# Kernel tuning notes

Hardware: AMD Instinct MI355X
Metric: run time of the kernel (lower is better)

The kernel has to match this reference:

```python
import jax, jax.numpy as jnp
import numpy as np

B, H, W, C = 8, 64, 64, 128
G = 8
K = 3
STRIDE, PAD, DIL = 1, 1, 1
OS = 1.0
HID = 2 * C
C_OUT = C
EPS = 1e-5


def setup_inputs():
    key = jax.random.key(0)
    ks = jax.random.split(key, 16)

    def n(k, shape, s=0.02):
        return jax.random.normal(k, shape, dtype=jnp.float32) * s

    inp = jax.random.normal(ks[0], (B, H, W, C), dtype=jnp.float32)
    return {
        "inp": inp,
        "w_proj": n(ks[1], (C, C), 0.05),
        "b_proj": jnp.zeros((C,), jnp.float32),
        "dw_w": n(ks[2], (C, 1, K, K), 0.1),
        "dw_b": jnp.zeros((C,), jnp.float32),
        "gamma": jnp.ones((C,), jnp.float32),
        "beta": jnp.zeros((C,), jnp.float32),
        "w_off": n(ks[3], (G * K * K * 2, C), 0.02),
        "b_off": n(ks[4], (G * K * K * 2,), 0.02),
        "w_mask": n(ks[5], (G * K * K, C), 0.02),
        "b_mask": n(ks[6], (G * K * K,), 0.02),
        "w_fc1": n(ks[7], (HID, C), 0.05),
        "b_fc1": jnp.zeros((HID,), jnp.float32),
        "w_fc2": n(ks[8], (C_OUT, HID), 0.05),
        "b_fc2": jnp.zeros((C_OUT,), jnp.float32),
    }


def _dcnv3_core(x, offset, mask):
    # x: (B,H,W,C); offset: (B,H,W,G*P*2); mask: (B,H,W,G*P), softmaxed over P
    b, h, w, c = x.shape
    cg = c // G
    p = K * K
    xpad = jnp.pad(x, ((0, 0), (PAD, PAD), (PAD, PAD), (0, 0)))
    hp, wp = h + 2 * PAD, w + 2 * PAD
    hout = (hp - (DIL * (K - 1) + 1)) // STRIDE + 1
    wout = (wp - (DIL * (K - 1) + 1)) // STRIDE + 1
    # reference points, normalized by padded spatial dims (DCNv3 convention)
    base = (DIL * (K - 1)) // 2 + 0.5
    ref_y = (base + jnp.arange(hout, dtype=x.dtype) * STRIDE) / hp
    ref_x = (base + jnp.arange(wout, dtype=x.dtype) * STRIDE) / wp
    # dilation kernel grid; flatten with p = i*K + j (row-major over kernel)
    k_lin = jnp.arange(K, dtype=x.dtype) * DIL - (DIL * (K - 1)) // 2
    grid_y = jnp.repeat(k_lin / hp, K)   # (P,)
    grid_x = jnp.tile(k_lin / wp, K)     # (P,)
    off = offset.reshape(b, hout, wout, G, p, 2)  # last dim = (dx, dy)
    loc_x = ref_x[None, None, :, None, None] + grid_x * OS + off[..., 0] * OS / wp
    loc_y = ref_y[None, :, None, None, None] + grid_y * OS + off[..., 1] * OS / hp
    # normalized [0,1] -> pixel coords (grid_sample align_corners=False)
    px = loc_x * wp - 0.5
    py = loc_y * hp - 0.5
    x0 = jnp.floor(px)
    y0 = jnp.floor(py)
    wx = px - x0
    wy = py - y0
    x0i = x0.astype(jnp.int32)
    y0i = y0.astype(jnp.int32)
    xg = xpad.reshape(b, hp * wp, G, cg).transpose(0, 2, 1, 3)  # (B,G,HpWp,Cg)
    m_tot = hout * wout * p

    def bgp(t):  # (B,Hout,Wout,G,P) -> (B,G,M,1)
        return t.transpose(0, 3, 1, 2, 4).reshape(b, G, m_tot)[..., None]

    def gather(iy, ix):
        valid = ((iy >= 0) & (iy < hp) & (ix >= 0) & (ix < wp)).astype(x.dtype)
        flat = jnp.clip(iy, 0, hp - 1) * wp + jnp.clip(ix, 0, wp - 1)
        v = jnp.take_along_axis(xg, bgp(flat), axis=2)  # (B,G,M,Cg)
        return v * bgp(valid)  # zero padding outside

    wxr, wyr = bgp(wx), bgp(wy)
    val = (gather(y0i, x0i) * (1 - wyr) * (1 - wxr)
           + gather(y0i, x0i + 1) * (1 - wyr) * wxr
           + gather(y0i + 1, x0i) * wyr * (1 - wxr)
           + gather(y0i + 1, x0i + 1) * wyr * wxr)
    m = bgp(mask.reshape(b, hout, wout, G, p))
    out = (val * m).reshape(b, G, hout * wout, p, cg).sum(3)  # (B,G,N,Cg)
    return out.transpose(0, 2, 1, 3).reshape(b, hout, wout, G * cg)


def reference(inp, w_proj, b_proj, dw_w, dw_b, gamma, beta, w_off, b_off,
              w_mask, b_mask, w_fc1, b_fc1, w_fc2, b_fc2):
    bsz = inp.shape[0]
    x = inp @ w_proj.T + b_proj  # input_proj
    # offset/mask branch: depthwise conv -> BN (batch stats) -> GELU
    xc = inp.transpose(0, 3, 1, 2)  # NCHW
    y = jax.lax.conv_general_dilated(
        xc, dw_w, (1, 1), [((K - 1) // 2, (K - 1) // 2)] * 2,
        feature_group_count=C, dimension_numbers=("NCHW", "OIHW", "NCHW"))
    y = y + dw_b[None, :, None, None]
    mean = y.mean(axis=(0, 2, 3), keepdims=True)
    var = ((y - mean) ** 2).mean(axis=(0, 2, 3), keepdims=True)
    y = (y - mean) * jax.lax.rsqrt(var + EPS)
    y = y * gamma[None, :, None, None] + beta[None, :, None, None]
    x1 = jax.nn.gelu(y, approximate=False).transpose(0, 2, 3, 1)  # (B,H,W,C)
    offset = x1 @ w_off.T + b_off
    mask = x1 @ w_mask.T + b_mask
    mask = jax.nn.softmax(mask.reshape(bsz, H, W, G, K * K), axis=-1).reshape(bsz, H, W, -1)
    x = _dcnv3_core(x, offset, mask)
    # out_proj MLP
    hdn = jax.nn.gelu(x @ w_fc1.T + b_fc1, approximate=False)
    out = hdn @ w_fc2.T + b_fc2
    return out.transpose(0, 3, 1, 2)  # (B,C_out,H,W)
```

## Files before the change

kernel.cpp:

```cpp
#include <hip/hip_runtime.h>
#include <math.h>

#define NPOS  32768
#define CDIM  128
#define HS    64
#define WSZ   64

typedef __bf16 bf8_t  __attribute__((ext_vector_type(8)));
typedef float  f32x4  __attribute__((ext_vector_type(4)));

__device__ __forceinline__ float gelu_exact(float x) {
    return 0.5f * x * (1.0f + erff(x * 0.70710678118654752f));
}

__device__ __forceinline__ unsigned short bf16c(float v) {
    return __builtin_bit_cast(unsigned short, (__bf16)v);
}

__device__ __forceinline__ uint4 pack8hi(const float* v) {
    unsigned hh[8];
    #pragma unroll
    for (int i = 0; i < 8; ++i) hh[i] = (unsigned)bf16c(v[i]);
    return make_uint4(hh[0] | (hh[1] << 16), hh[2] | (hh[3] << 16),
                      hh[4] | (hh[5] << 16), hh[6] | (hh[7] << 16));
}

__device__ __forceinline__ float bfd(unsigned u) {
    return __builtin_bit_cast(float, u << 16);
}

__device__ __forceinline__ void ufma(float* acc, uint4 c, float wgt) {
    const unsigned* cc = (const unsigned*)&c;
    #pragma unroll
    for (int j = 0; j < 4; ++j) {
        acc[2 * j]     += __builtin_bit_cast(float, cc[j] << 16) * wgt;
        acc[2 * j + 1] += __builtin_bit_cast(float, cc[j] & 0xFFFF0000u) * wgt;
    }
}


__device__ void prep_body(
    int bid, int tid,
    unsigned short* __restrict__ xpad,
    const float* __restrict__ w0, const float* __restrict__ w1,
    const float* __restrict__ w2, const float* __restrict__ w3,
    const float* __restrict__ w4, unsigned short* __restrict__ wb)
{
    if (bid < 130) {
        int idx = bid * 256 + tid;
        if (idx < 33280) {
            int c8 = (idx & 15) * 8;
            int cell = idx >> 4;
            int b = cell / 260, r = cell % 260;
            int h, w;
            if (r < 66)       { h = 0;  w = r; }
            else if (r < 132) { h = 65; w = r - 66; }
            else { int rr = r - 132; h = 1 + (rr >> 1); w = (rr & 1) * 65; }
            size_t o = (((size_t)b * 66 + h) * 66 + w) * 128 + c8;
            *(uint4*)(xpad + o) = make_uint4(0u, 0u, 0u, 0u);
        }
    } else {
        int sub = (bid - 130) * 4 + (tid >> 6);
        int lane = tid & 63;
        int NT, K, local; unsigned short* out; bool hl; bool comb = false;
        const float* W = nullptr; int N = 0;
        if (sub < 32)       { NT = 8;  K = 128; out = wb;          local = sub;       hl = false; W = w0; N = 128; }
        else if (sub < 88)  { NT = 14; K = 128; out = wb + 16384;  local = sub - 32;  hl = false; comb = true; }
        else if (sub < 152) { NT = 16; K = 128; out = wb + 45056;  local = sub - 88;  hl = true;  W = w3; N = 256; }
        else                { NT = 8;  K = 256; out = wb + 110592; local = sub - 152; hl = true;  W = w4; N = 128; }
        int KC = K / 32;
        int unit = KC * NT * 512;
        int kc = local / NT, t = local % NT;
        int nt = t * 16 + (lane & 15);
        const float* Wp = W; int n = nt, Nv = N;
        if (comb) {
            if (t < 9) { Wp = w1; n = nt;       Nv = 144; }
            else       { Wp = w2; n = nt - 144; Nv = 72;  }
        }
        int kb = kc * 32 + (lane >> 4) * 8;
        size_t base = ((size_t)local * 64 + lane) * 8;
        #pragma unroll
        for (int i = 0; i < 8; ++i) {
            float v = (n < Nv) ? Wp[(size_t)n * K + kb + i] : 0.f;
            __bf16 h = (__bf16)v;
            out[base + i] = __builtin_bit_cast(unsigned short, h);
            if (hl) {
                __bf16 l = (__bf16)(v - (float)h);
                out[unit + base + i] = __builtin_bit_cast(unsigned short, l);
            }
        }
    }
}

__device__ void dwconv_body(
    int blk, int tid,
    const float* __restrict__ inp, const float* __restrict__ dww,
    const float* __restrict__ dwb, unsigned short* __restrict__ ydwb,
    float* __restrict__ psum, float* __restrict__ psq,
    unsigned short* __restrict__ inpf)
{
    int b = blk >> 6, h = blk & 63;
    int c4 = (tid & 31) * 4;
    int wg = tid >> 5;

    float wreg[4][9];
    #pragma unroll
    for (int cc = 0; cc < 4; ++cc)
        #pragma unroll
        for (int p = 0; p < 9; ++p)
            wreg[cc][p] = dww[(c4 + cc) * 9 + p];
    float bia[4];
    #pragma unroll
    for (int cc = 0; cc < 4; ++cc) bia[cc] = dwb[c4 + cc];

    float s4[4] = {0,0,0,0}, q4[4] = {0,0,0,0};
    const float* ibase = inp + (size_t)(b << 12) * CDIM;

    for (int i = 0; i < 8; ++i) {
        int w = wg + i * 8;
        float acc[4] = {bia[0], bia[1], bia[2], bia[3]};
        float4 ctr;
        #pragma unroll
        for (int ky = 0; ky < 3; ++ky) {
            int yy = h + ky - 1;
            if (yy < 0 || yy >= HS) continue;
            #pragma unroll
            for (int kx = 0; kx < 3; ++kx) {
                int xx = w + kx - 1;
                if (xx < 0 || xx >= WSZ) continue;
                float4 v = *(const float4*)(ibase + (size_t)(yy * 64 + xx) * CDIM + c4);
                if (ky == 1 && kx == 1) ctr = v;
                int p = ky * 3 + kx;
                acc[0] += v.x * wreg[0][p];
                acc[1] += v.y * wreg[1][p];
                acc[2] += v.z * wreg[2][p];
                acc[3] += v.w * wreg[3][p];
            }
        }
        int r = (b << 12) + h * 64 + w;
        ushort4 o;
        o.x = bf16c(acc[0]); o.y = bf16c(acc[1]);
        o.z = bf16c(acc[2]); o.w = bf16c(acc[3]);
        *(ushort4*)(ydwb + (size_t)r * CDIM + c4) = o;
        {
            int rt = r >> 4, kc = c4 >> 5;
            int lp = (r & 15) + ((c4 & 31) >> 3) * 16;
            int i0 = c4 & 7;
            unsigned u0 = (unsigned)bf16c(ctr.x) | ((unsigned)bf16c(ctr.y) << 16);
            unsigned u1 = (unsigned)bf16c(ctr.z) | ((unsigned)bf16c(ctr.w) << 16);
            *(uint2*)(inpf + ((size_t)rt * 4 + kc) * 512 + lp * 8 + i0) = make_uint2(u0, u1);
        }
        #pragma unroll
        for (int cc = 0; cc < 4; ++cc) { s4[cc] += acc[cc]; q4[cc] += acc[cc] * acc[cc]; }
    }

    __shared__ float ls[8][128], lq[8][128];
    #pragma unroll
    for (int cc = 0; cc < 4; ++cc) { ls[wg][c4 + cc] = s4[cc]; lq[wg][c4 + cc] = q4[cc]; }
    __syncthreads();
    if (tid < 128) {
        float s = 0.f, q = 0.f;
        #pragma unroll
        for (int r = 0; r < 8; ++r) { s += ls[r][tid]; q += lq[r][tid]; }
        psum[blk * 128 + tid] = s;
        psq [blk * 128 + tid] = q;
    }
}

__global__ __launch_bounds__(256) void k_pd(
    const float* __restrict__ inp, unsigned short* __restrict__ inpf,
    unsigned short* __restrict__ xpad,
    const float* __restrict__ w0, const float* __restrict__ w1,
    const float* __restrict__ w2, const float* __restrict__ w3,
    const float* __restrict__ w4, unsigned short* __restrict__ wb,
    const float* __restrict__ dww, const float* __restrict__ dwb,
    unsigned short* __restrict__ ydwb, float* __restrict__ psum,
    float* __restrict__ psq)
{
    int bid = blockIdx.x;
    if (bid < 184) prep_body(bid, threadIdx.x, xpad, w0, w1, w2, w3, w4, wb);
    else           dwconv_body(bid - 184, threadIdx.x, inp, dww, dwb, ydwb, psum, psq, inpf);
}

__global__ __launch_bounds__(256) void k_bnstats(
    const float* __restrict__ psum, const float* __restrict__ psq,
    const float* __restrict__ gamma, const float* __restrict__ beta,
    float* __restrict__ sc, float* __restrict__ sh)
{
    int c = blockIdx.x;
    int t = threadIdx.x;
    float s = psum[t * 128 + c] + psum[(t + 256) * 128 + c];
    float q = psq [t * 128 + c] + psq [(t + 256) * 128 + c];
    __shared__ float rs[256], rq[256];
    rs[t] = s; rq[t] = q; __syncthreads();
    for (int off = 128; off > 0; off >>= 1) {
        if (t < off) { rs[t] += rs[t + off]; rq[t] += rq[t + off]; }
        __syncthreads();
    }
    if (t == 0) {
        float mean = rs[0] * (1.0f / 32768.0f);
        float var  = rq[0] * (1.0f / 32768.0f) - mean * mean;
        float scale = gamma[c] * rsqrtf(var + 1e-5f);
        sc[c] = scale;
        sh[c] = beta[c] - mean * scale;
    }
}

__device__ void bngelu_body(
    int bid, int tid,
    const unsigned short* __restrict__ ydwb, const float* __restrict__ sc,
    const float* __restrict__ sh, unsigned short* __restrict__ dst)
{
    int idx = bid * 256 + tid;
    int r = idx >> 4, k8 = (idx & 15) * 8;
    uint4 yv = *(const uint4*)(ydwb + (size_t)r * 128 + k8);
    const unsigned* cc = (const unsigned*)&yv;
    float t[8];
    #pragma unroll
    for (int j = 0; j < 4; ++j) {
        t[2 * j]     = bfd(cc[j]);
        t[2 * j + 1] = __builtin_bit_cast(float, cc[j] & 0xFFFF0000u);
    }
    float s[8], h[8];
    *(float4*)(s)     = *(const float4*)(sc + k8);
    *(float4*)(s + 4) = *(const float4*)(sc + k8 + 4);
    *(float4*)(h)     = *(const float4*)(sh + k8);
    *(float4*)(h + 4) = *(const float4*)(sh + k8 + 4);
    #pragma unroll
    for (int i = 0; i < 8; ++i) t[i] = gelu_exact(t[i] * s[i] + h[i]);
    uint4 hi = pack8hi(t);
    int rt = r >> 4, kc = k8 >> 5, lp = (r & 15) + ((k8 & 31) >> 3) * 16;
    size_t base = ((size_t)rt * 4 + kc) * 512 + lp * 8;
    *(uint4*)(dst + base) = hi;
}

template<int KDIM, int NT_TOT, int NT_W, int MODE, int NV>
__device__ void fgemm_body(
    int bx, int by, int tid,
    const unsigned short* __restrict__ AF, const unsigned short* __restrict__ WF,
    const float* __restrict__ bias, float* __restrict__ C)
{
    constexpr int KC = KDIM / 32;
    int lane = tid & 63, w = tid >> 6;
    int rt0 = bx * 8 + w * 2;
    int t0 = by * NT_W;

    f32x4 acc[2][NT_W];
    #pragma unroll
    for (int rt = 0; rt < 2; ++rt)
        #pragma unroll
        for (int t = 0; t < NT_W; ++t) acc[rt][t] = (f32x4){0.f, 0.f, 0.f, 0.f};

    const bf8_t* Ab0 = (const bf8_t*)AF + (size_t)rt0 * KC * 64 + lane;
    const bf8_t* Ab1 = Ab0 + KC * 64;
    const bf8_t* WHp = (const bf8_t*)WF + lane;

    #pragma unroll
    for (int kc = 0; kc < KC; ++kc) {
        bf8_t a0h = Ab0[kc * 64];
        bf8_t a1h = Ab1[kc * 64];
        #pragma unroll
        for (int t = 0; t < NT_W; ++t) {
            int tg = t0 + t;
            if (tg < NT_TOT) {
                bf8_t wh = WHp[(kc * NT_TOT + tg) * 64];
                acc[0][t] = __builtin_amdgcn_mfma_f32_16x16x32_bf16(wh, a0h, acc[0][t], 0, 0, 0);
                acc[1][t] = __builtin_amdgcn_mfma_f32_16x16x32_bf16(wh, a1h, acc[1][t], 0, 0, 0);
            }
        }
    }

    #pragma unroll
    for (int rt = 0; rt < 2; ++rt) {
        if (MODE == 3) {
            unsigned short* Cp = (unsigned short*)C;
            int m = (rt0 + rt) * 16 + (lane & 15);
            int bb_ = m >> 12, hwm = m & 4095;
            size_t rowb = (((size_t)bb_ * 66 + (hwm >> 6) + 1) * 66 + (hwm & 63) + 1) * 128;
            #pragma unroll
            for (int t = 0; t < NT_W; ++t) {
                int tg = t0 + t;
                int nb = tg * 16 + ((lane >> 4) << 2);
                if (tg < NT_TOT) {
                    float4 bb = *(const float4*)(bias + nb);
                    f32x4 a = acc[rt][t];
                    ushort4 v;
                    v.x = bf16c(a[0] + bb.x); v.y = bf16c(a[1] + bb.y);
                    v.z = bf16c(a[2] + bb.z); v.w = bf16c(a[3] + bb.w);
                    *(ushort4*)(Cp + rowb + nb) = v;
                }
            }
        }
    }
}

__global__ __launch_bounds__(256) void k_bp(
    const unsigned short* __restrict__ ydwb, const float* __restrict__ sc,
    const float* __restrict__ sh, unsigned short* __restrict__ x1f,
    const unsigned short* __restrict__ inpf, const unsigned short* __restrict__ wprojf,
    const float* __restrict__ bproj, unsigned short* __restrict__ xpad)
{
    int bid = blockIdx.x;
    if (bid < 2048) {
        bngelu_body(bid, threadIdx.x, ydwb, sc, sh, x1f);
    } else {
        int pbid = bid - 2048;
        fgemm_body<128, 8, 4, 3, 128>(pbid & 255, pbid >> 8, threadIdx.x,
            inpf, wprojf, bproj, (float*)xpad);
    }
}

__global__ __launch_bounds__(512) void k_dcn(
    const unsigned short* __restrict__ x1f, const unsigned short* __restrict__ womb,
    const float* __restrict__ boff, const float* __restrict__ bmask,
    const unsigned short* __restrict__ xpad, unsigned short* __restrict__ dcnf)
{
    __shared__ unsigned short offs_l[32][148];
    __shared__ unsigned short msk_l[32][76];
    int tid = threadIdx.x;
    int lane = tid & 63, wv = tid >> 6;
    int rtl = wv & 1, chunk = wv >> 1;
    int rt = blockIdx.x * 2 + rtl;

    {
        f32x4 acc[4];
        #pragma unroll
        for (int t = 0; t < 4; ++t) acc[t] = (f32x4){0.f, 0.f, 0.f, 0.f};
        const bf8_t* Ab = (const bf8_t*)x1f + (size_t)rt * 4 * 64 + lane;
        const bf8_t* WH = (const bf8_t*)womb + lane;
        #pragma unroll
        for (int kc = 0; kc < 4; ++kc) {
            bf8_t ah = Ab[kc * 64];
            #pragma unroll
            for (int t = 0; t < 4; ++t) {
                int tg = chunk * 4 + t;
                if (tg < 14) {
                    bf8_t wh = WH[(kc * 14 + tg) * 64];
                    acc[t] = __builtin_amdgcn_mfma_f32_16x16x32_bf16(wh, ah, acc[t], 0, 0, 0);
                }
            }
        }
        int m = rtl * 16 + (lane & 15);
        #pragma unroll
        for (int t = 0; t < 4; ++t) {
            int tg = chunk * 4 + t;
            if (tg < 14) {
                int nb = tg * 16 + ((lane >> 4) << 2);
                f32x4 a = acc[t];
                if (nb < 144) {
                    float4 bb = *(const float4*)(boff + nb);
                    ushort4 v;
                    v.x = bf16c(a[0] + bb.x); v.y = bf16c(a[1] + bb.y);
                    v.z = bf16c(a[2] + bb.z); v.w = bf16c(a[3] + bb.w);
                    *(ushort4*)(&offs_l[m][nb]) = v;
                } else {
                    int col = nb - 144;
                    if (col + 4 <= 72) {
                        float4 bb = *(const float4*)(bmask + col);
                        ushort4 v;
                        v.x = bf16c(a[0] + bb.x); v.y = bf16c(a[1] + bb.y);
                        v.z = bf16c(a[2] + bb.z); v.w = bf16c(a[3] + bb.w);
                        *(ushort4*)(&msk_l[m][col]) = v;
                    }
                }
            }
        }
    }
    __syncthreads();

    int q = tid & 1;
    int g = (tid >> 1) & 7;
    int lpos = tid >> 4;
    int pos = blockIdx.x * 32 + lpos;
    int b = pos >> 12, hw = pos & 4095, h = hw >> 6, w = hw & 63;

    float e[9];
    float mx = -1e30f;
    #pragma unroll
    for (int p = 0; p < 9; ++p) { e[p] = bfd((unsigned)msk_l[lpos][g * 9 + p]); mx = fmaxf(mx, e[p]); }
    float ssum = 0.f;
    #pragma unroll
    for (int p = 0; p < 9; ++p) { e[p] = __expf(e[p] - mx); ssum += e[p]; }
    float inv = 1.0f / ssum;

    int ch = g * 16 + q * 8;
    const unsigned short* xb = xpad + (size_t)b * 557568 + ch;

    float acc[8];
    #pragma unroll
    for (int i = 0; i < 8; ++i) acc[i] = 0.f;

    #pragma unroll
    for (int p = 0; p < 9; ++p) {
        unsigned dpair = *(const unsigned*)(&offs_l[lpos][g * 18 + p * 2]);
        float dx = bfd(dpair);
        float dy = __builtin_bit_cast(float, dpair & 0xFFFF0000u);
        float px = (float)(w + (p % 3)) + dx;
        float py = (float)(h + (p / 3)) + dy;
        float x0f = floorf(px), y0f = floorf(py);
        float wx = px - x0f, wy = py - y0f;
        int ix = (int)x0f, iy = (int)y0f;
        int ix0 = max(min(ix, 65), 0),     ix1 = max(min(ix + 1, 65), 0);
        int iy0 = max(min(iy, 65), 0),     iy1 = max(min(iy + 1, 65), 0);
        int r0 = iy0 * 66, r1 = iy1 * 66;

        float mp  = e[p] * inv;
        float w11 = wy * wx * mp;
        float w10 = wy * mp - w11;
        float w01 = wx * mp - w11;
        float w00 = mp - w01 - w10 - w11;

        uint4 s00 = *(const uint4*)(xb + (size_t)(r0 + ix0) * 128);
        uint4 s01 = *(const uint4*)(xb + (size_t)(r0 + ix1) * 128);
        uint4 s10 = *(const uint4*)(xb + (size_t)(r1 + ix0) * 128);
        uint4 s11 = *(const uint4*)(xb + (size_t)(r1 + ix1) * 128);

        ufma(acc, s00, w00);
        ufma(acc, s01, w01);
        ufma(acc, s10, w10);
        ufma(acc, s11, w11);
    }

    int rto = pos >> 4, kc = ch >> 5;
    int lp = (pos & 15) + (((g & 1) << 1) + q) * 16;
    size_t fb = ((size_t)rto * 4 + kc) * 512 + (size_t)lp * 8;
    *(uint4*)(dcnf + fb) = pack8hi(acc);
}

__global__ __launch_bounds__(512) void k_mlp(
    const unsigned short* __restrict__ dcnf, const unsigned short* __restrict__ wf1,
    const float* __restrict__ bfc1, const unsigned short* __restrict__ wf2,
    const float* __restrict__ bfc2, float* __restrict__ out)
{
    __shared__ unsigned short hid[4][16][264];
    int tid = threadIdx.x;
    int lane = tid & 63, w = tid >> 6;
    int pr = w & 1, chunk = w >> 1;
    int bp = blockIdx.x * 2 + pr;
    int rt0 = bp * 2;
    int m = lane & 15, hi4 = (lane >> 4) << 2;

    f32x4 acc[2][4];
    #pragma unroll
    for (int r = 0; r < 2; ++r)
        #pragma unroll
        for (int t = 0; t < 4; ++t) acc[r][t] = (f32x4){0.f, 0.f, 0.f, 0.f};
    const bf8_t* Ab0 = (const bf8_t*)dcnf + (size_t)rt0 * 4 * 64 + lane;
    const bf8_t* Ab1 = Ab0 + 4 * 64;
    const bf8_t* WH1 = (const bf8_t*)wf1 + lane;
    #pragma unroll
    for (int kc = 0; kc < 4; ++kc) {
        bf8_t a0 = Ab0[kc * 64];
        bf8_t a1 = Ab1[kc * 64];
        #pragma unroll
        for (int t = 0; t < 4; ++t) {
            int tg = chunk * 4 + t;
            bf8_t wh = WH1[(kc * 16 + tg) * 64];
            acc[0][t] = __builtin_amdgcn_mfma_f32_16x16x32_bf16(wh, a0, acc[0][t], 0, 0, 0);
            acc[1][t] = __builtin_amdgcn_mfma_f32_16x16x32_bf16(wh, a1, acc[1][t], 0, 0, 0);
        }
    }
    #pragma unroll
    for (int r = 0; r < 2; ++r) {
        #pragma unroll
        for (int t = 0; t < 4; ++t) {
            int nb = (chunk * 4 + t) * 16 + hi4;
            float4 bb = *(const float4*)(bfc1 + nb);
            ushort4 v;
            v.x = bf16c(gelu_exact(acc[r][t][0] + bb.x));
            v.y = bf16c(gelu_exact(acc[r][t][1] + bb.y));
            v.z = bf16c(gelu_exact(acc[r][t][2] + bb.z));
            v.w = bf16c(gelu_exact(acc[r][t][3] + bb.w));
            *(ushort4*)(&hid[pr * 2 + r][m][nb]) = v;
        }
    }

    __syncthreads();

    f32x4 acc2[2][2];
    #pragma unroll
    for (int r = 0; r < 2; ++r)
        #pragma unroll
        for (int t = 0; t < 2; ++t) acc2[r][t] = (f32x4){0.f, 0.f, 0.f, 0.f};
    const bf8_t* WH2 = (const bf8_t*)wf2 + lane;
    #pragma unroll
    for (int kc = 0; kc < 8; ++kc) {
        bf8_t ah0 = *(const bf8_t*)(&hid[pr * 2 + 0][m][kc * 32 + (lane >> 4) * 8]);
        bf8_t ah1 = *(const bf8_t*)(&hid[pr * 2 + 1][m][kc * 32 + (lane >> 4) * 8]);
        #pragma unroll
        for (int t = 0; t < 2; ++t) {
            int tg = chunk * 2 + t;
            bf8_t wh = WH2[(kc * 8 + tg) * 64];
            acc2[0][t] = __builtin_amdgcn_mfma_f32_16x16x32_bf16(ah0, wh, acc2[0][t], 0, 0, 0);
            acc2[1][t] = __builtin_amdgcn_mfma_f32_16x16x32_bf16(ah1, wh, acc2[1][t], 0, 0, 0);
        }
    }
    #pragma unroll
    for (int r = 0; r < 2; ++r) {
        int m4 = (rt0 + r) * 16 + hi4;
        int b = m4 >> 12, hw = m4 & 4095;
        #pragma unroll
        for (int t = 0; t < 2; ++t) {
            int n = (chunk * 2 + t) * 16 + m;
            float bb = bfc2[n];
            f32x4 a = acc2[r][t];
            float4 v = {a[0] + bb, a[1] + bb, a[2] + bb, a[3] + bb};
            *(float4*)(out + (((size_t)(b * 128 + n)) << 12) + hw) = v;
        }
    }
}

extern "C" void kernel_launch(void* const* d_in, const int* in_sizes, int n_in,
                              void* d_out, int out_size, void* d_ws, size_t ws_size,
                              hipStream_t stream)
{
    const float* inp   = (const float*)d_in[0];
    const float* wproj = (const float*)d_in[1];
    const float* bproj = (const float*)d_in[2];
    const float* dww   = (const float*)d_in[3];
    const float* dwb   = (const float*)d_in[4];
    const float* gamma = (const float*)d_in[5];
    const float* beta  = (const float*)d_in[6];
    const float* woff  = (const float*)d_in[7];
    const float* boff  = (const float*)d_in[8];
    const float* wmask = (const float*)d_in[9];
    const float* bmask = (const float*)d_in[10];
    const float* wfc1  = (const float*)d_in[11];
    const float* bfc1  = (const float*)d_in[12];
    const float* wfc2  = (const float*)d_in[13];
    const float* bfc2  = (const float*)d_in[14];
    float* out = (float*)d_out;
    float* ws  = (float*)d_ws;

    unsigned short* xpad = (unsigned short*)ws;
    unsigned short* inpf  = (unsigned short*)(ws + 9179136);
    unsigned short* dcnf  = (unsigned short*)(ws + 9179136);
    unsigned short* x1f   = (unsigned short*)(ws + 13373440);
    unsigned short* ydwb  = (unsigned short*)(ws + 15470592);
    float* psum = ws + 19927040;
    float* psq  = ws + 19992576;
    float* scs  = ws + 20058112;
    float* shs  = ws + 20058240;
    unsigned short* wfr = (unsigned short*)(ws + 20058368);

    unsigned short* wproj_f = wfr;
    unsigned short* womb_f  = wfr + 16384;
    unsigned short* wfc1_f  = wfr + 45056;
    unsigned short* wfc2_f  = wfr + 110592;

    k_pd<<<696, 256, 0, stream>>>(inp, inpf, xpad, wproj, woff, wmask, wfc1, wfc2,
                                  wfr, dww, dwb, ydwb, psum, psq);
    k_bnstats<<<128, 256, 0, stream>>>(psum, psq, gamma, beta, scs, shs);
    k_bp<<<2560, 256, 0, stream>>>(ydwb, scs, shs, x1f, inpf, wproj_f, bproj, xpad);
    k_dcn<<<1024, 512, 0, stream>>>(x1f, womb_f, boff, bmask, xpad, dcnf);
    k_mlp<<<512, 512, 0, stream>>>(dcnf, wfc1_f, bfc1, wfc2_f, bfc2, out);
}
```

Before: 82.51 us.

## Fuse deformable sampling and output MLP into one kernel via shared memory

Merges the DCN sampling kernel and the two-layer MLP kernel into a single kernel. The sampled features for each 32-position block stay in shared memory and feed the fc1/fc2 MFMA stages directly, which removes the dcnf global round trip and one launch. Shared memory is aliased between the offset/mask staging and the hidden buffer. In exchange, each block now covers only 32 rows, so fc weights are reloaded by twice as many blocks, and two extra barriers are added.

```diff
diff --git a/kernel.cpp b/kernel.cpp
--- a/kernel.cpp
+++ b/kernel.cpp
@@ -310,17 +310,24 @@
     }
 }
 
-__global__ __launch_bounds__(512) void k_dcn(
+__global__ __launch_bounds__(512) void k_dm(
     const unsigned short* __restrict__ x1f, const unsigned short* __restrict__ womb,
     const float* __restrict__ boff, const float* __restrict__ bmask,
-    const unsigned short* __restrict__ xpad, unsigned short* __restrict__ dcnf)
-{
-    __shared__ unsigned short offs_l[32][148];
-    __shared__ unsigned short msk_l[32][76];
+    const unsigned short* __restrict__ xpad,
+    const unsigned short* __restrict__ wf1, const float* __restrict__ bfc1,
+    const unsigned short* __restrict__ wf2, const float* __restrict__ bfc2,
+    float* __restrict__ out)
+{
+    __shared__ unsigned short hid[2][16][264];
+    __shared__ unsigned short dcn_l[2][16][136];
+    unsigned short (*offs_l)[148] = (unsigned short (*)[148])(&hid[0][0][0]);
+    unsigned short (*msk_l)[76]   = (unsigned short (*)[76])(&hid[0][0][0] + 4736);
+
     int tid = threadIdx.x;
     int lane = tid & 63, wv = tid >> 6;
     int rtl = wv & 1, chunk = wv >> 1;
     int rt = blockIdx.x * 2 + rtl;
+    int m = lane & 15, hi4 = (lane >> 4) << 2;
 
     {
         f32x4 acc[4];
@@ -340,19 +347,19 @@
                 }
             }
         }
-        int m = rtl * 16 + (lane & 15);
+        int ml = rtl * 16 + m;
         #pragma unroll
         for (int t = 0; t < 4; ++t) {
             int tg = chunk * 4 + t;
             if (tg < 14) {
-                int nb = tg * 16 + ((lane >> 4) << 2);
+                int nb = tg * 16 + hi4;
                 f32x4 a = acc[t];
                 if (nb < 144) {
                     float4 bb = *(const float4*)(boff + nb);
                     ushort4 v;
                     v.x = bf16c(a[0] + bb.x); v.y = bf16c(a[1] + bb.y);
                     v.z = bf16c(a[2] + bb.z); v.w = bf16c(a[3] + bb.w);
-                    *(ushort4*)(&offs_l[m][nb]) = v;
+                    *(ushort4*)(&offs_l[ml][nb]) = v;
                 } else {
                     int col = nb - 144;
                     if (col + 4 <= 72) {
@@ -360,7 +367,7 @@
                         ushort4 v;
                         v.x = bf16c(a[0] + bb.x); v.y = bf16c(a[1] + bb.y);
                         v.z = bf16c(a[2] + bb.z); v.w = bf16c(a[3] + bb.w);
-                        *(ushort4*)(&msk_l[m][col]) = v;
+                        *(ushort4*)(&msk_l[ml][col]) = v;
                     }
                 }
             }
@@ -368,142 +375,115 @@
     }
     __syncthreads();
 
-    int q = tid & 1;
-    int g = (tid >> 1) & 7;
-    int lpos = tid >> 4;
-    int pos = blockIdx.x * 32 + lpos;
-    int b = pos >> 12, hw = pos & 4095, h = hw >> 6, w = hw & 63;
-
-    float e[9];
-    float mx = -1e30f;
-    #pragma unroll
-    for (int p = 0; p < 9; ++p) { e[p] = bfd((unsigned)msk_l[lpos][g * 9 + p]); mx = fmaxf(mx, e[p]); }
-    float ssum = 0.f;
-    #pragma unroll
-    for (int p = 0; p < 9; ++p) { e[p] = __expf(e[p] - mx); ssum += e[p]; }
-    float inv = 1.0f / ssum;
-
-    int ch = g * 16 + q * 8;
-    const unsigned short* xb = xpad + (size_t)b * 557568 + ch;
-
-    float acc[8];
-    #pragma unroll
-    for (int i = 0; i < 8; ++i) acc[i] = 0.f;
-
-    #pragma unroll
-    for (int p = 0; p < 9; ++p) {
-        unsigned dpair = *(const unsigned*)(&offs_l[lpos][g * 18 + p * 2]);
-        float dx = bfd(dpair);
-        float dy = __builtin_bit_cast(float, dpair & 0xFFFF0000u);
-        float px = (float)(w + (p % 3)) + dx;
-        float py = (float)(h + (p / 3)) + dy;
-        float x0f = floorf(px), y0f = floorf(py);
-        float wx = px - x0f, wy = py - y0f;
-        int ix = (int)x0f, iy = (int)y0f;
-        int ix0 = max(min(ix, 65), 0),     ix1 = max(min(ix + 1, 65), 0);
-        int iy0 = max(min(iy, 65), 0),     iy1 = max(min(iy + 1, 65), 0);
-        int r0 = iy0 * 66, r1 = iy1 * 66;
-
-        float mp  = e[p] * inv;
-        float w11 = wy * wx * mp;
-        float w10 = wy * mp - w11;
-        float w01 = wx * mp - w11;
-        float w00 = mp - w01 - w10 - w11;
-
-        uint4 s00 = *(const uint4*)(xb + (size_t)(r0 + ix0) * 128);
-        uint4 s01 = *(const uint4*)(xb + (size_t)(r0 + ix1) * 128);
-        uint4 s10 = *(const uint4*)(xb + (size_t)(r1 + ix0) * 128);
-        uint4 s11 = *(const uint4*)(xb + (size_t)(r1 + ix1) * 128);
-
-        ufma(acc, s00, w00);
-        ufma(acc, s01, w01);
-        ufma(acc, s10, w10);
-        ufma(acc, s11, w11);
-    }
-
-    int rto = pos >> 4, kc = ch >> 5;
-    int lp = (pos & 15) + (((g & 1) << 1) + q) * 16;
-    size_t fb = ((size_t)rto * 4 + kc) * 512 + (size_t)lp * 8;
-    *(uint4*)(dcnf + fb) = pack8hi(acc);
-}
-
-__global__ __launch_bounds__(512) void k_mlp(
-    const unsigned short* __restrict__ dcnf, const unsigned short* __restrict__ wf1,
-    const float* __restrict__ bfc1, const unsigned short* __restrict__ wf2,
-    const float* __restrict__ bfc2, float* __restrict__ out)
-{
-    __shared__ unsigned short hid[4][16][264];
-    int tid = threadIdx.x;
-    int lane = tid & 63, w = tid >> 6;
-    int pr = w & 1, chunk = w >> 1;
-    int bp = blockIdx.x * 2 + pr;
-    int rt0 = bp * 2;
-    int m = lane & 15, hi4 = (lane >> 4) << 2;
-
-    f32x4 acc[2][4];
-    #pragma unroll
-    for (int r = 0; r < 2; ++r)
-        #pragma unroll
-        for (int t = 0; t < 4; ++t) acc[r][t] = (f32x4){0.f, 0.f, 0.f, 0.f};
-    const bf8_t* Ab0 = (const bf8_t*)dcnf + (size_t)rt0 * 4 * 64 + lane;
-    const bf8_t* Ab1 = Ab0 + 4 * 64;
-    const bf8_t* WH1 = (const bf8_t*)wf1 + lane;
-    #pragma unroll
-    for (int kc = 0; kc < 4; ++kc) {
-        bf8_t a0 = Ab0[kc * 64];
-        bf8_t a1 = Ab1[kc * 64];
-        #pragma unroll
-        for (int t = 0; t < 4; ++t) {
-            int tg = chunk * 4 + t;
-            bf8_t wh = WH1[(kc * 16 + tg) * 64];
-            acc[0][t] = __builtin_amdgcn_mfma_f32_16x16x32_bf16(wh, a0, acc[0][t], 0, 0, 0);
-            acc[1][t] = __builtin_amdgcn_mfma_f32_16x16x32_bf16(wh, a1, acc[1][t], 0, 0, 0);
-        }
-    }
-    #pragma unroll
-    for (int r = 0; r < 2; ++r) {
+    {
+        int q = tid & 1;
+        int g = (tid >> 1) & 7;
+        int lpos = tid >> 4;
+        int pos = blockIdx.x * 32 + lpos;
+        int b = pos >> 12, hw = pos & 4095, h = hw >> 6, w = hw & 63;
+
+        float e[9];
+        float mx = -1e30f;
+        #pragma unroll
+        for (int p = 0; p < 9; ++p) { e[p] = bfd((unsigned)msk_l[lpos][g * 9 + p]); mx = fmaxf(mx, e[p]); }
+        float ssum = 0.f;
+        #pragma unroll
+        for (int p = 0; p < 9; ++p) { e[p] = __expf(e[p] - mx); ssum += e[p]; }
+        float inv = 1.0f / ssum;
+
+        int ch = g * 16 + q * 8;
+        const unsigned short* xb = xpad + (size_t)b * 557568 + ch;
+
+        float acc[8];
+        #pragma unroll
+        for (int i = 0; i < 8; ++i) acc[i] = 0.f;
+
+        #pragma unroll
+        for (int p = 0; p < 9; ++p) {
+            unsigned dpair = *(const unsigned*)(&offs_l[lpos][g * 18 + p * 2]);
+            float dx = bfd(dpair);
+            float dy = __builtin_bit_cast(float, dpair & 0xFFFF0000u);
+            float px = (float)(w + (p % 3)) + dx;
+            float py = (float)(h + (p / 3)) + dy;
+            float x0f = floorf(px), y0f = floorf(py);
+            float wx = px - x0f, wy = py - y0f;
+            int ix = (int)x0f, iy = (int)y0f;
+            int ix0 = max(min(ix, 65), 0),     ix1 = max(min(ix + 1, 65), 0);
+            int iy0 = max(min(iy, 65), 0),     iy1 = max(min(iy + 1, 65), 0);
+            int r0 = iy0 * 66, r1 = iy1 * 66;
+
+            float mp  = e[p] * inv;
+            float w11 = wy * wx * mp;
+            float w10 = wy * mp - w11;
+            float w01 = wx * mp - w11;
+            float w00 = mp - w01 - w10 - w11;
+
+            uint4 s00 = *(const uint4*)(xb + (size_t)(r0 + ix0) * 128);
+            uint4 s01 = *(const uint4*)(xb + (size_t)(r0 + ix1) * 128);
+            uint4 s10 = *(const uint4*)(xb + (size_t)(r1 + ix0) * 128);
+            uint4 s11 = *(const uint4*)(xb + (size_t)(r1 + ix1) * 128);
+
+            ufma(acc, s00, w00);
+            ufma(acc, s01, w01);
+            ufma(acc, s10, w10);
+            ufma(acc, s11, w11);
+        }
+
+        *(uint4*)(&dcn_l[lpos >> 4][lpos & 15][ch]) = pack8hi(acc);
+    }
+    __syncthreads();
+
+    {
+        f32x4 acc[4];
+        #pragma unroll
+        for (int t = 0; t < 4; ++t) acc[t] = (f32x4){0.f, 0.f, 0.f, 0.f};
+        const bf8_t* WH1 = (const bf8_t*)wf1 + lane;
+        #pragma unroll
+        for (int kc = 0; kc < 4; ++kc) {
+            bf8_t ah = *(const bf8_t*)(&dcn_l[rtl][m][kc * 32 + (lane >> 4) * 8]);
+            #pragma unroll
+            for (int t = 0; t < 4; ++t) {
+                int tg = chunk * 4 + t;
+                bf8_t wh = WH1[(kc * 16 + tg) * 64];
+                acc[t] = __builtin_amdgcn_mfma_f32_16x16x32_bf16(wh, ah, acc[t], 0, 0, 0);
+            }
+        }
         #pragma unroll
         for (int t = 0; t < 4; ++t) {
             int nb = (chunk * 4 + t) * 16 + hi4;
             float4 bb = *(const float4*)(bfc1 + nb);
             ushort4 v;
-            v.x = bf16c(gelu_exact(acc[r][t][0] + bb.x));
-            v.y = bf16c(gelu_exact(acc[r][t][1] + bb.y));
-            v.z = bf16c(gelu_exact(acc[r][t][2] + bb.z));
-            v.w = bf16c(gelu_exact(acc[r][t][3] + bb.w));
-            *(ushort4*)(&hid[pr * 2 + r][m][nb]) = v;
-        }
-    }
-
+            v.x = bf16c(gelu_exact(acc[t][0] + bb.x));
+            v.y = bf16c(gelu_exact(acc[t][1] + bb.y));
+            v.z = bf16c(gelu_exact(acc[t][2] + bb.z));
+            v.w = bf16c(gelu_exact(acc[t][3] + bb.w));
+            *(ushort4*)(&hid[rtl][m][nb]) = v;
+        }
+    }
     __syncthreads();
 
-    f32x4 acc2[2][2];
-    #pragma unroll
-    for (int r = 0; r < 2; ++r)
-        #pragma unroll
-        for (int t = 0; t < 2; ++t) acc2[r][t] = (f32x4){0.f, 0.f, 0.f, 0.f};
-    const bf8_t* WH2 = (const bf8_t*)wf2 + lane;
-    #pragma unroll
-    for (int kc = 0; kc < 8; ++kc) {
-        bf8_t ah0 = *(const bf8_t*)(&hid[pr * 2 + 0][m][kc * 32 + (lane >> 4) * 8]);
-        bf8_t ah1 = *(const bf8_t*)(&hid[pr * 2 + 1][m][kc * 32 + (lane >> 4) * 8]);
-        #pragma unroll
-        for (int t = 0; t < 2; ++t) {
-            int tg = chunk * 2 + t;
-            bf8_t wh = WH2[(kc * 8 + tg) * 64];
-            acc2[0][t] = __builtin_amdgcn_mfma_f32_16x16x32_bf16(ah0, wh, acc2[0][t], 0, 0, 0);
-            acc2[1][t] = __builtin_amdgcn_mfma_f32_16x16x32_bf16(ah1, wh, acc2[1][t], 0, 0, 0);
-        }
-    }
-    #pragma unroll
-    for (int r = 0; r < 2; ++r) {
-        int m4 = (rt0 + r) * 16 + hi4;
+    {
+        f32x4 acc2[2];
+        #pragma unroll
+        for (int t = 0; t < 2; ++t) acc2[t] = (f32x4){0.f, 0.f, 0.f, 0.f};
+        const bf8_t* WH2 = (const bf8_t*)wf2 + lane;
+        #pragma unroll
+        for (int kc = 0; kc < 8; ++kc) {
+            bf8_t ah = *(const bf8_t*)(&hid[rtl][m][kc * 32 + (lane >> 4) * 8]);
+            #pragma unroll
+            for (int t = 0; t < 2; ++t) {
+                int tg = chunk * 2 + t;
+                bf8_t wh = WH2[(kc * 8 + tg) * 64];
+                acc2[t] = __builtin_amdgcn_mfma_f32_16x16x32_bf16(ah, wh, acc2[t], 0, 0, 0);
+            }
+        }
+        int m4 = rt * 16 + hi4;
         int b = m4 >> 12, hw = m4 & 4095;
         #pragma unroll
         for (int t = 0; t < 2; ++t) {
             int n = (chunk * 2 + t) * 16 + m;
             float bb = bfc2[n];
-            f32x4 a = acc2[r][t];
+            f32x4 a = acc2[t];
             float4 v = {a[0] + bb, a[1] + bb, a[2] + bb, a[3] + bb};
             *(float4*)(out + (((size_t)(b * 128 + n)) << 12) + hw) = v;
         }
@@ -534,7 +514,6 @@
 
     unsigned short* xpad = (unsigned short*)ws;
     unsigned short* inpf  = (unsigned short*)(ws + 9179136);
-    unsigned short* dcnf  = (unsigned short*)(ws + 9179136);
     unsigned short* x1f   = (unsigned short*)(ws + 13373440);
     unsigned short* ydwb  = (unsigned short*)(ws + 15470592);
     float* psum = ws + 19927040;
@@ -552,6 +531,6 @@
                                   wfr, dww, dwb, ydwb, psum, psq);
     k_bnstats<<<128, 256, 0, stream>>>(psum, psq, gamma, beta, scs, shs);
     k_bp<<<2560, 256, 0, stream>>>(ydwb, scs, shs, x1f, inpf, wproj_f, bproj, xpad);
-    k_dcn<<<1024, 512, 0, stream>>>(x1f, womb_f, boff, bmask, xpad, dcnf);
-    k_mlp<<<512, 512, 0, stream>>>(dcnf, wfc1_f, bfc1, wfc2_f, bfc2, out);
-}
+    k_dm<<<1024, 512, 0, stream>>>(x1f, womb_f, boff, bmask, xpad,
+                                   wfc1_f, bfc1, wfc2_f, bfc2, out);
+}
```

Result: slower. 90.70 us (+9.9%).
